# Performance work log

Measured on AMD Instinct MI355X. Metric: run time of the kernel, lower is better.

The kernel has to match this reference:

```python
import jax, jax.numpy as jnp
import numpy as np

B, D, T, R = 8, 128, 32768, 2
C = D // R  # reduced channel dim = 64


def conv1x1(x, w, b):
    # x: [B, Cin, T], w: [Cout, Cin], b: [Cout] -> [B, Cout, T]
    return jnp.einsum('oi,bit->bot', w, x) + b[None, :, None]


def setup_inputs() -> dict:
    key = jax.random.key(0)
    ks = jax.random.split(key, 16)
    inp = {
        'x1': jax.random.normal(ks[0], (B, D, T), dtype=jnp.float32),
        'x2': jnp.zeros((B, D, T), dtype=jnp.float32),  # unused in encoder stage
        'mask': jnp.ones((B, 1, T), dtype=jnp.float32),
        # 1x1 conv projections (weights squeezed to [out, in])
        'wq': jax.random.normal(ks[1], (C, D), dtype=jnp.float32) * 0.05,
        'bq': jnp.zeros((C,), dtype=jnp.float32),
        'wk': jax.random.normal(ks[2], (C, D), dtype=jnp.float32) * 0.05,
        'bk': jnp.zeros((C,), dtype=jnp.float32),
        'wv': jax.random.normal(ks[3], (C, D), dtype=jnp.float32) * 0.05,
        'bv': jnp.zeros((C,), dtype=jnp.float32),
        # E, F: Linear(C -> C) with bias
        'we': jax.random.normal(ks[4], (C, C), dtype=jnp.float32) * 0.1,
        'be': jnp.zeros((C,), dtype=jnp.float32),
        'wf': jax.random.normal(ks[5], (C, C), dtype=jnp.float32) * 0.1,
        'bf': jnp.zeros((C,), dtype=jnp.float32),
        # output 1x1 conv: C -> D
        'wo': jax.random.normal(ks[6], (D, C), dtype=jnp.float32) * 0.05,
        'bo': jnp.zeros((D,), dtype=jnp.float32),
    }
    return inp


def reference(x1, x2, mask, wq, bq, wk, bk, wv, bv, we, be, wf, bf, wo, bo):
    # Q/K/V projections (encoder stage: value from x1; x2 unused)
    Q = conv1x1(x1, wq, bq)              # [B, C, T]
    K = conv1x1(x1, wk, bk)              # [B, C, T]
    V = conv1x1(x1, wv, bv)              # [B, C, T]
    # K = E(K^T): [B, T, C] @ we^T + be
    Kp = jnp.einsum('bct,oc->bto', K, we) + be  # [B, T, C]
    # S = Q @ Kp -> [B, C, C], scaled by sqrt(last dim)
    S = jnp.einsum('bct,btk->bck', Q, Kp)
    P = jax.nn.softmax(S / jnp.sqrt(jnp.asarray(S.shape[-1], S.dtype)), axis=-1)
    # dropout is identity in eval mode
    # V = (F(V^T))^T: [B, C, T]
    Vp = jnp.einsum('bct,oc->bot', V, wf) + bf[None, :, None]  # [B, C, T]
    out = jnp.einsum('bck,bkt->bct', P, Vp)  # [B, C, T]
    out = conv1x1(jax.nn.relu(out), wo, bo)  # [B, D, T]
    return out * mask[:, 0:1, :]
```

## Files before the change

### kernel.cpp

```cpp
#include <hip/hip_runtime.h>
#include <stdint.h>
#include <stddef.h>

#define B_ 8
#define D_ 128
#define T_ 32768
#define C_ 64
#define NCH_ 64

typedef __bf16 bf16;
typedef __bf16 bf16x4 __attribute__((ext_vector_type(4)));
typedef __bf16 bf16x8 __attribute__((ext_vector_type(8)));
typedef float f32x4 __attribute__((ext_vector_type(4)));
typedef float f32x16 __attribute__((ext_vector_type(16)));

__device__ __forceinline__ f32x16 zero16() {
  f32x16 z;
#pragma unroll
  for (int i = 0; i < 16; ++i) z[i] = 0.f;
  return z;
}

__global__ __launch_bounds__(256) void k0_zero(float* __restrict__ p, int n)
{
  int i = blockIdx.x * 256 + threadIdx.x;
  if (i < n) p[i] = 0.f;
}

__global__ __launch_bounds__(256, 4) void k1_gram(
    const float* __restrict__ x1,
    const float* __restrict__ we, const float* __restrict__ wk,
    const float* __restrict__ bk, const float* __restrict__ be,
    const float* __restrict__ wf, const float* __restrict__ wv,
    const float* __restrict__ bv, const float* __restrict__ bfv,
    const float* __restrict__ wo,
    float* __restrict__ G, float* __restrict__ r,
    float* __restrict__ wkp, float* __restrict__ wvp,
    float* __restrict__ bkp, float* __restrict__ bvp,
    bf16* __restrict__ wobf,
    float* __restrict__ gpart)
{
  const int blk = blockIdx.x;
  const int tid = threadIdx.x;
  const int ngram = B_ * NCH_;

  if (blk >= ngram) {
    const int wb = blk - ngram;
    if (wb < 64) {
      const float* wa  = (wb < 32) ? we : wf;
      const float* wb2 = (wb < 32) ? wk : wv;
      float* outw      = (wb < 32) ? wkp : wvp;
      const int idx = (wb & 31) * 256 + tid;
      const int o = idx >> 7, d = idx & 127;
      float s = 0.f;
      for (int c = 0; c < 64; ++c) s += wa[o * 64 + c] * wb2[c * 128 + d];
      outw[idx] = s;
      if (tid < 64) {
        if (wb == 0) {
          float t = 0.f;
          for (int c = 0; c < 64; ++c) t += we[tid * 64 + c] * bk[c];
          bkp[tid] = t + be[tid];
        } else if (wb == 32) {
          float t = 0.f;
          for (int c = 0; c < 64; ++c) t += wf[tid * 64 + c] * bv[c];
          bvp[tid] = t + bfv[tid];
        }
      }
    } else {
      const int idx = (wb - 64) * 256 + tid;
      wobf[idx] = (bf16)wo[idx];
    }
    return;
  }

  __shared__ bf16 x_s[128 * 72];

  const int b  = blk / NCH_;
  const int ch = blk & (NCH_ - 1);
  const int t0 = ch * (T_ / NCH_);
  const int wave = tid >> 6, lane = tid & 63;
  const int lrow = lane & 31, lk = lane >> 5;
  const int qa = wave >> 1, qb = wave & 1;

  const float* xb = x1 + (size_t)b * D_ * T_;

  f32x16 acc00 = zero16(), acc01 = zero16(), acc10 = zero16(), acc11 = zero16();
  float rsum = 0.f;

  const int scol = (tid & 15) * 4;
  const int srow0 = tid >> 4;

  const bf16* A0  = &x_s[(64 * qa + lrow) * 72 + 8 * lk];
  const bf16* A1  = A0 + 32 * 72;
  const bf16* Bb0 = &x_s[(64 * qb + lrow) * 72 + 8 * lk];
  const bf16* Bb1 = Bb0 + 32 * 72;

  for (int s = 0; s < 8; ++s) {
    const int tb = t0 + s * 64;
    if (s) __syncthreads();
#pragma unroll
    for (int it = 0; it < 8; ++it) {
      const int row = it * 16 + srow0;
      f32x4 v = *(const f32x4*)(xb + (size_t)row * T_ + tb + scol);
      bf16x4 h;
#pragma unroll
      for (int j = 0; j < 4; ++j) h[j] = (bf16)v[j];
      *(bf16x4*)&x_s[row * 72 + scol] = h;
    }
    __syncthreads();
#pragma unroll
    for (int k = 0; k < 4; ++k) {
      bf16x8 fa0 = *(const bf16x8*)(A0 + 16 * k);
      bf16x8 fa1 = *(const bf16x8*)(A1 + 16 * k);
      bf16x8 fb0 = *(const bf16x8*)(Bb0 + 16 * k);
      bf16x8 fb1 = *(const bf16x8*)(Bb1 + 16 * k);
      bf16x8 own = qb ? fa1 : fa0;
#pragma unroll
      for (int j = 0; j < 8; ++j) rsum += (float)own[j];
      acc00 = __builtin_amdgcn_mfma_f32_32x32x16_bf16(fa0, fb0, acc00, 0, 0, 0);
      acc01 = __builtin_amdgcn_mfma_f32_32x32x16_bf16(fa0, fb1, acc01, 0, 0, 0);
      acc10 = __builtin_amdgcn_mfma_f32_32x32x16_bf16(fa1, fb0, acc10, 0, 0, 0);
      acc11 = __builtin_amdgcn_mfma_f32_32x32x16_bf16(fa1, fb1, acc11, 0, 0, 0);
    }
  }

  if (gpart) {
    float* gp = gpart + (size_t)blk * 16384;
#pragma unroll
    for (int rr = 0; rr < 16; ++rr) {
      const int rloc = (rr & 3) + 8 * (rr >> 2) + 4 * lk;
      const int r0 = 64 * qa + rloc, r1 = 64 * qa + 32 + rloc;
      const int c0 = 64 * qb + lrow, c1 = 64 * qb + 32 + lrow;
      gp[r0 * 128 + c0] = acc00[rr];
      gp[r0 * 128 + c1] = acc01[rr];
      gp[r1 * 128 + c0] = acc10[rr];
      gp[r1 * 128 + c1] = acc11[rr];
    }
  } else {
    float* gb = G + (size_t)b * 16384;
#pragma unroll
    for (int rr = 0; rr < 16; ++rr) {
      const int rloc = (rr & 3) + 8 * (rr >> 2) + 4 * lk;
      const int r0 = 64 * qa + rloc, r1 = 64 * qa + 32 + rloc;
      const int c0 = 64 * qb + lrow, c1 = 64 * qb + 32 + lrow;
      atomicAdd(&gb[r0 * 128 + c0], acc00[rr]);
      atomicAdd(&gb[r0 * 128 + c1], acc01[rr]);
      atomicAdd(&gb[r1 * 128 + c0], acc10[rr]);
      atomicAdd(&gb[r1 * 128 + c1], acc11[rr]);
    }
  }
  float rtot = rsum + __shfl_xor(rsum, 32, 64);
  if (lk == 0) atomicAdd(&r[b * 128 + 32 * wave + lrow], rtot);
}

__global__ __launch_bounds__(256) void k2_reduce(
    const float* __restrict__ gpart, float* __restrict__ G)
{
  const int g4 = blockIdx.x * 256 + threadIdx.x;
  const int b = g4 >> 12;
  const int e4 = g4 & 4095;
  const f32x4* p = (const f32x4*)(gpart + ((size_t)b * NCH_) * 16384) + e4;
  f32x4 s = {0.f, 0.f, 0.f, 0.f};
#pragma unroll
  for (int ch = 0; ch < NCH_; ++ch) s += p[(size_t)ch * 4096];
  *((f32x4*)G + g4) = s;
}

__global__ __launch_bounds__(128) void k3_softmax(
    const float* __restrict__ wq, const float* __restrict__ bq,
    const float* __restrict__ G, const float* __restrict__ r,
    const float* __restrict__ wkp, const float* __restrict__ wvp,
    const float* __restrict__ bkp, const float* __restrict__ bvp,
    bf16* __restrict__ attw, float* __restrict__ attb)
{
  const int b = blockIdx.x >> 6, c = blockIdx.x & 63;
  const int tid = threadIdx.x;
  __shared__ float sM[128], sR[128], sQ[128], sP[64];
  __shared__ float sRed;

  const float* Gb = G + (size_t)b * 16384;
  const float* wqc = wq + c * 128;

  const float rv = r[b * 128 + tid];
  sR[tid] = rv;
  float m = 0.f;
  for (int j = 0; j < 128; ++j) m += wqc[j] * Gb[j * 128 + tid];
  sM[tid] = m;
  sQ[tid] = wqc[tid] * rv;
  __syncthreads();

  if (tid < 64) {
    float q2 = sQ[tid] + sQ[tid + 64];
#pragma unroll
    for (int off = 32; off; off >>= 1) q2 += __shfl_xor(q2, off, 64);
    if (tid == 0) sRed = q2;
  }
  __syncthreads();
  const float qr = sRed;
  const float bqc = bq[c];

  if (tid < 64) {
    const int k = tid;
    float s = 0.f, wkr = 0.f;
    for (int i = 0; i < 128; ++i) {
      const float w = wkp[k * 128 + i];
      s += sM[i] * w;
      wkr += sR[i] * w;
    }
    const float bk2 = bkp[k];
    float logit = (s + bqc * wkr + bk2 * qr + (float)T_ * bqc * bk2) * 0.125f;
    float mx = logit;
#pragma unroll
    for (int off = 32; off; off >>= 1) mx = fmaxf(mx, __shfl_xor(mx, off, 64));
    const float e = __expf(logit - mx);
    float sum = e;
#pragma unroll
    for (int off = 32; off; off >>= 1) sum += __shfl_xor(sum, off, 64);
    sP[k] = e / sum;
  }
  __syncthreads();

  {
    float aw = 0.f;
    for (int k = 0; k < 64; ++k) aw += sP[k] * wvp[k * 128 + tid];
    attw[((size_t)b * 64 + c) * 128 + tid] = (bf16)aw;
  }
  if (tid < 64) {
    float pb = sP[tid] * bvp[tid];
#pragma unroll
    for (int off = 32; off; off >>= 1) pb += __shfl_xor(pb, off, 64);
    if (tid == 0) attb[b * 64 + c] = pb;
  }
}

__global__ __launch_bounds__(256, 4) void k4_out(
    const float* __restrict__ x1, const float* __restrict__ mask,
    const bf16* __restrict__ wobf, const float* __restrict__ bo,
    const bf16* __restrict__ attw, const float* __restrict__ attb,
    float* __restrict__ out)
{
  __shared__ bf16 m1[128 * 72];
  __shared__ float bo_s[128];
  __shared__ float ab_s[64];

  const int b = blockIdx.x >> 8;
  const int t0 = (blockIdx.x & 255) << 7;
  const int tid = threadIdx.x;
  const int wave = tid >> 6, lane = tid & 63;
  const int lrow = lane & 31, lk = lane >> 5;
  const int tcol = 32 * wave + lrow;

  if (tid < 128) bo_s[tid] = bo[tid];
  if (tid < 64) ab_s[tid] = attb[b * 64 + tid];
  __syncthreads();

  const float* xc = x1 + (size_t)b * D_ * T_ + t0 + tcol;
  const bf16* awb = attw + (size_t)b * 8192;

  f32x16 p0 = zero16(), p1 = zero16();
#pragma unroll
  for (int k0 = 0; k0 < 8; ++k0) {
    bf16x8 a0 = *(const bf16x8*)(awb + (size_t)lrow * 128 + 16 * k0 + 8 * lk);
    bf16x8 a1 = *(const bf16x8*)(awb + (size_t)(32 + lrow) * 128 + 16 * k0 + 8 * lk);
    bf16x8 bx;
#pragma unroll
    for (int j = 0; j < 8; ++j)
      bx[j] = (bf16)xc[(size_t)(16 * k0 + 8 * lk + j) * T_];
    p0 = __builtin_amdgcn_mfma_f32_32x32x16_bf16(a0, bx, p0, 0, 0, 0);
    p1 = __builtin_amdgcn_mfma_f32_32x32x16_bf16(a1, bx, p1, 0, 0, 0);
  }
  bf16* mrow = &m1[tcol * 72];
#pragma unroll
  for (int rr = 0; rr < 16; ++rr) {
    const int row = (rr & 3) + 8 * (rr >> 2) + 4 * lk;
    mrow[row]      = (bf16)fmaxf(p0[rr] + ab_s[row], 0.f);
    mrow[32 + row] = (bf16)fmaxf(p1[rr] + ab_s[32 + row], 0.f);
  }

  f32x16 q0 = zero16(), q1 = zero16(), q2 = zero16(), q3 = zero16();
#pragma unroll
  for (int k0 = 0; k0 < 4; ++k0) {
    bf16x8 bm = *(const bf16x8*)(mrow + 16 * k0 + 8 * lk);
    bf16x8 w0 = *(const bf16x8*)(wobf + (size_t)(lrow) * 64 + 16 * k0 + 8 * lk);
    bf16x8 w1 = *(const bf16x8*)(wobf + (size_t)(32 + lrow) * 64 + 16 * k0 + 8 * lk);
    bf16x8 w2 = *(const bf16x8*)(wobf + (size_t)(64 + lrow) * 64 + 16 * k0 + 8 * lk);
    bf16x8 w3 = *(const bf16x8*)(wobf + (size_t)(96 + lrow) * 64 + 16 * k0 + 8 * lk);
    q0 = __builtin_amdgcn_mfma_f32_32x32x16_bf16(w0, bm, q0, 0, 0, 0);
    q1 = __builtin_amdgcn_mfma_f32_32x32x16_bf16(w1, bm, q1, 0, 0, 0);
    q2 = __builtin_amdgcn_mfma_f32_32x32x16_bf16(w2, bm, q2, 0, 0, 0);
    q3 = __builtin_amdgcn_mfma_f32_32x32x16_bf16(w3, bm, q3, 0, 0, 0);
  }

  const float mv = mask[(size_t)b * T_ + t0 + tcol];
  float* ob = out + (size_t)b * D_ * T_ + t0 + tcol;
#pragma unroll
  for (int rr = 0; rr < 16; ++rr) {
    const int row = (rr & 3) + 8 * (rr >> 2) + 4 * lk;
    ob[(size_t)(row) * T_]      = (q0[rr] + bo_s[row]) * mv;
    ob[(size_t)(32 + row) * T_] = (q1[rr] + bo_s[32 + row]) * mv;
    ob[(size_t)(64 + row) * T_] = (q2[rr] + bo_s[64 + row]) * mv;
    ob[(size_t)(96 + row) * T_] = (q3[rr] + bo_s[96 + row]) * mv;
  }
}

extern "C" void kernel_launch(void* const* d_in, const int* in_sizes, int n_in,
                              void* d_out, int out_size, void* d_ws, size_t ws_size,
                              hipStream_t stream)
{
  const float* x1   = (const float*)d_in[0];
  const float* mask = (const float*)d_in[2];
  const float* wq   = (const float*)d_in[3];
  const float* bq   = (const float*)d_in[4];
  const float* wk   = (const float*)d_in[5];
  const float* bk   = (const float*)d_in[6];
  const float* wv   = (const float*)d_in[7];
  const float* bv   = (const float*)d_in[8];
  const float* we   = (const float*)d_in[9];
  const float* be   = (const float*)d_in[10];
  const float* wf   = (const float*)d_in[11];
  const float* bfv  = (const float*)d_in[12];
  const float* wo   = (const float*)d_in[13];
  const float* bo   = (const float*)d_in[14];
  float* out = (float*)d_out;

  char* base = (char*)d_ws;
  size_t off = 0;
  float* G    = (float*)(base + off); off += (size_t)B_ * 16384 * 4;
  float* r    = (float*)(base + off); off += (size_t)B_ * 128 * 4;
  float* wkp  = (float*)(base + off); off += 8192 * 4;
  float* wvp  = (float*)(base + off); off += 8192 * 4;
  float* bkp  = (float*)(base + off); off += 64 * 4;
  float* bvp  = (float*)(base + off); off += 64 * 4;
  float* attb = (float*)(base + off); off += (size_t)B_ * 64 * 4;
  bf16* attw  = (bf16*)(base + off);  off += (size_t)B_ * 64 * 128 * 2;
  bf16* wobf  = (bf16*)(base + off);  off += 8192 * 2;
  off = (off + 15) & ~(size_t)15;
  float* gpart = (float*)(base + off);
  const size_t need = off + (size_t)B_ * NCH_ * 16384 * 4;
  const bool use_part = (ws_size >= need);
  if (!use_part) gpart = nullptr;

  const int nzero = B_ * 16384 + B_ * 128;
  k0_zero<<<(nzero + 255) / 256, 256, 0, stream>>>(G, nzero);
  k1_gram<<<B_ * NCH_ + 96, 256, 0, stream>>>(
      x1, we, wk, bk, be, wf, wv, bv, bfv, wo,
      G, r, wkp, wvp, bkp, bvp, wobf, gpart);
  if (use_part)
    k2_reduce<<<(B_ * 16384) / (256 * 4), 256, 0, stream>>>(gpart, G);
  k3_softmax<<<B_ * 64, 128, 0, stream>>>(wq, bq, G, r, wkp, wvp, bkp, bvp, attw, attb);
  k4_out<<<B_ * (T_ / 128), 256, 0, stream>>>(x1, mask, wobf, bo, attw, attb, out);
}
```

Before: 380.7 us.

## Cache bf16 copy of x in gram pass, prefetch loads, shrink zero-init

The gram kernel now software-pipelines its global loads by prefetching the next 64-column chunk into registers while the current chunk is consumed by MFMA. It also writes a bf16 copy of x1 to workspace, so the output kernel reads half the bytes instead of re-reading fp32 x1. When partial sums are used, only the row-sum buffer is zeroed rather than all of G, and the reduce loop unroll is capped at 8. The trade-off is an extra 64 MB write in the gram pass and higher register pressure from the prefetch buffers.

```diff
diff --git a/kernel.cpp b/kernel.cpp
--- a/kernel.cpp
+++ b/kernel.cpp
@@ -38,7 +38,7 @@
     float* __restrict__ wkp, float* __restrict__ wvp,
     float* __restrict__ bkp, float* __restrict__ bvp,
     bf16* __restrict__ wobf,
-    float* __restrict__ gpart)
+    float* __restrict__ gpart, bf16* __restrict__ xbf)
 {
   const int blk = blockIdx.x;
   const int tid = threadIdx.x;
@@ -83,6 +83,7 @@
   const int qa = wave >> 1, qb = wave & 1;
 
   const float* xb = x1 + (size_t)b * D_ * T_;
+  bf16* xo = xbf ? (xbf + (size_t)b * D_ * T_ + t0) : nullptr;
 
   f32x16 acc00 = zero16(), acc01 = zero16(), acc10 = zero16(), acc11 = zero16();
   float rsum = 0.f;
@@ -95,19 +96,33 @@
   const bf16* Bb0 = &x_s[(64 * qb + lrow) * 72 + 8 * lk];
   const bf16* Bb1 = Bb0 + 32 * 72;
 
+  f32x4 pre[8];
+#pragma unroll
+  for (int it = 0; it < 8; ++it) {
+    const int row = it * 16 + srow0;
+    pre[it] = *(const f32x4*)(xb + (size_t)row * T_ + t0 + scol);
+  }
+
   for (int s = 0; s < 8; ++s) {
-    const int tb = t0 + s * 64;
     if (s) __syncthreads();
 #pragma unroll
     for (int it = 0; it < 8; ++it) {
       const int row = it * 16 + srow0;
-      f32x4 v = *(const f32x4*)(xb + (size_t)row * T_ + tb + scol);
       bf16x4 h;
 #pragma unroll
-      for (int j = 0; j < 4; ++j) h[j] = (bf16)v[j];
+      for (int j = 0; j < 4; ++j) h[j] = (bf16)pre[it][j];
       *(bf16x4*)&x_s[row * 72 + scol] = h;
+      if (xo) *(bf16x4*)(xo + (size_t)row * T_ + s * 64 + scol) = h;
     }
     __syncthreads();
+    if (s < 7) {
+      const int tb = t0 + (s + 1) * 64;
+#pragma unroll
+      for (int it = 0; it < 8; ++it) {
+        const int row = it * 16 + srow0;
+        pre[it] = *(const f32x4*)(xb + (size_t)row * T_ + tb + scol);
+      }
+    }
 #pragma unroll
     for (int k = 0; k < 4; ++k) {
       bf16x8 fa0 = *(const bf16x8*)(A0 + 16 * k);
@@ -161,7 +176,7 @@
   const int e4 = g4 & 4095;
   const f32x4* p = (const f32x4*)(gpart + ((size_t)b * NCH_) * 16384) + e4;
   f32x4 s = {0.f, 0.f, 0.f, 0.f};
-#pragma unroll
+#pragma unroll 8
   for (int ch = 0; ch < NCH_; ++ch) s += p[(size_t)ch * 4096];
   *((f32x4*)G + g4) = s;
 }
@@ -234,7 +249,8 @@
 }
 
 __global__ __launch_bounds__(256, 4) void k4_out(
-    const float* __restrict__ x1, const float* __restrict__ mask,
+    const float* __restrict__ x1, const bf16* __restrict__ xbf,
+    const float* __restrict__ mask,
     const bf16* __restrict__ wobf, const float* __restrict__ bo,
     const bf16* __restrict__ attw, const float* __restrict__ attb,
     float* __restrict__ out)
@@ -255,6 +271,7 @@
   __syncthreads();
 
   const float* xc = x1 + (size_t)b * D_ * T_ + t0 + tcol;
+  const bf16* xbc = xbf ? (xbf + (size_t)b * D_ * T_ + t0 + tcol) : nullptr;
   const bf16* awb = attw + (size_t)b * 8192;
 
   f32x16 p0 = zero16(), p1 = zero16();
@@ -263,9 +280,15 @@
     bf16x8 a0 = *(const bf16x8*)(awb + (size_t)lrow * 128 + 16 * k0 + 8 * lk);
     bf16x8 a1 = *(const bf16x8*)(awb + (size_t)(32 + lrow) * 128 + 16 * k0 + 8 * lk);
     bf16x8 bx;
-#pragma unroll
-    for (int j = 0; j < 8; ++j)
-      bx[j] = (bf16)xc[(size_t)(16 * k0 + 8 * lk + j) * T_];
+    if (xbc) {
+#pragma unroll
+      for (int j = 0; j < 8; ++j)
+        bx[j] = xbc[(size_t)(16 * k0 + 8 * lk + j) * T_];
+    } else {
+#pragma unroll
+      for (int j = 0; j < 8; ++j)
+        bx[j] = (bf16)xc[(size_t)(16 * k0 + 8 * lk + j) * T_];
+    }
     p0 = __builtin_amdgcn_mfma_f32_32x32x16_bf16(a0, bx, p0, 0, 0, 0);
     p1 = __builtin_amdgcn_mfma_f32_32x32x16_bf16(a1, bx, p1, 0, 0, 0);
   }
@@ -336,17 +359,27 @@
   bf16* wobf  = (bf16*)(base + off);  off += 8192 * 2;
   off = (off + 15) & ~(size_t)15;
   float* gpart = (float*)(base + off);
-  const size_t need = off + (size_t)B_ * NCH_ * 16384 * 4;
-  const bool use_part = (ws_size >= need);
-  if (!use_part) gpart = nullptr;
-
-  const int nzero = B_ * 16384 + B_ * 128;
-  k0_zero<<<(nzero + 255) / 256, 256, 0, stream>>>(G, nzero);
+  const size_t off_gp = off + (size_t)B_ * NCH_ * 16384 * 4;
+  bf16* xbf = (bf16*)(base + off_gp);
+  const size_t need_full = off_gp + (size_t)B_ * D_ * T_ * 2;
+
+  bool use_part = true, use_xbf = true;
+  if (ws_size < need_full) use_xbf = false;
+  if (ws_size < off_gp)    use_part = false;
+  if (!use_part) { gpart = nullptr; }
+  if (!use_xbf)  { xbf = nullptr; }
+
+  if (use_part) {
+    k0_zero<<<(B_ * 128 + 255) / 256, 256, 0, stream>>>(r, B_ * 128);
+  } else {
+    const int nzero = B_ * 16384 + B_ * 128;
+    k0_zero<<<(nzero + 255) / 256, 256, 0, stream>>>(G, nzero);
+  }
   k1_gram<<<B_ * NCH_ + 96, 256, 0, stream>>>(
       x1, we, wk, bk, be, wf, wv, bv, bfv, wo,
-      G, r, wkp, wvp, bkp, bvp, wobf, gpart);
+      G, r, wkp, wvp, bkp, bvp, wobf, gpart, xbf);
   if (use_part)
     k2_reduce<<<(B_ * 16384) / (256 * 4), 256, 0, stream>>>(gpart, G);
   k3_softmax<<<B_ * 64, 128, 0, stream>>>(wq, bq, G, r, wkp, wvp, bkp, bvp, attw, attb);
-  k4_out<<<B_ * (T_ / 128), 256, 0, stream>>>(x1, mask, wobf, bo, attw, attb, out);
-}
+  k4_out<<<B_ * (T_ / 128), 256, 0, stream>>>(x1, xbf, mask, wobf, bo, attw, attb, out);
+}
```

New measurement: 396.2 us. 4.1% more time.
